# Kernel tuning notes

Measured on AMD Instinct MI355X. Metric: run time of the kernel, lower is better.

Reference implementation:

```python
import math
import jax, jax.numpy as jnp
import numpy as np


def setup_inputs() -> dict:
    key = jax.random.key(0)
    ks = jax.random.split(key, 6)
    B, L, d_model = 8, 4096, 512
    s = 1.0 / math.sqrt(d_model)
    inp = {
        "x": jax.random.normal(ks[0], (B, L, d_model), dtype=jnp.float32),
        "Wq": jax.random.normal(ks[1], (d_model, d_model), dtype=jnp.float32) * s,
        "bq": jnp.zeros((d_model,), jnp.float32),
        "Wk": jax.random.normal(ks[2], (d_model, d_model), dtype=jnp.float32) * s,
        "bk": jnp.zeros((d_model,), jnp.float32),
        "Wv": jax.random.normal(ks[3], (d_model, d_model), dtype=jnp.float32) * s,
        "bv": jnp.zeros((d_model,), jnp.float32),
        "Wo": jax.random.normal(ks[4], (d_model, d_model), dtype=jnp.float32) * s,
        "bo": jnp.zeros((d_model,), jnp.float32),
    }
    return inp


N_HEADS = 8
FACTOR = 1


def reference(x, Wq, bq, Wk, bk, Wv, bv, Wo, bo):
    B, L, d_model = x.shape
    H = N_HEADS
    D = d_model // H
    # projections (torch Linear: x @ W.T + b), reshape to (B,H,L,D)
    def proj(W, b):
        y = jnp.einsum("bld,ed->ble", x, W) + b
        return y.reshape(B, L, H, D).transpose(0, 2, 1, 3)
    q = proj(Wq, bq)
    k = proj(Wk, bk)
    v = proj(Wv, bv)
    # FFT autocorrelation along time axis (axis=2)
    q_f = jnp.fft.rfft(q, axis=2)
    k_f = jnp.fft.rfft(k, axis=2)
    corr = jnp.fft.irfft(q_f * jnp.conj(k_f), n=L, axis=2)  # (B,H,L,D)
    k_top = max(1, int(FACTOR * math.log(L + 1)))
    k_top = min(k_top, L)
    corr_mean = corr.mean(axis=-1)  # (B,H,L)
    top_vals, top_idx = jax.lax.top_k(corr_mean, k_top)  # (B,H,k)
    weights = jax.nn.softmax(top_vals, axis=-1)  # (B,H,k)
    t = jnp.arange(L).reshape(1, 1, 1, L)
    idx = (t + top_idx[..., None]) % L  # (B,H,k,L)
    # gather rolled V per selected lag: (B,H,k,L,D)
    v_exp = jnp.broadcast_to(v[:, :, None], (B, H, k_top, L, D))
    gathered = jnp.take_along_axis(v_exp, idx[..., None], axis=3)
    out = jnp.einsum("bhkld,bhk->bhld", gathered, weights)
    out = out.transpose(0, 2, 1, 3).reshape(B, L, d_model)
    # dropout=0.0 (eval): identity
    return jnp.einsum("bld,ed->ble", out, Wo) + bo
```

## Files before the change

kernel.cpp:

```cpp
#include <hip/hip_runtime.h>
#include <cstdint>
#include <cstddef>

#define AS1 __attribute__((address_space(1)))
#define AS3 __attribute__((address_space(3)))

using half8  = __attribute__((ext_vector_type(8))) _Float16;
using half4v = __attribute__((ext_vector_type(4))) _Float16;
using half2v = __attribute__((ext_vector_type(2))) _Float16;
using f32x4  = __attribute__((ext_vector_type(4))) float;

__global__ void prep_all_kernel(const float* __restrict__ x,
                                const float* __restrict__ Wq, const float* __restrict__ Wk,
                                const float* __restrict__ Wv, const float* __restrict__ Wo,
                                const float* __restrict__ bq, const float* __restrict__ bk,
                                const float* __restrict__ bv,
                                _Float16* __restrict__ xh, _Float16* __restrict__ Bt,
                                _Float16* __restrict__ WoH,
                                float2* __restrict__ tw, float* __restrict__ bias) {
    const int bid = blockIdx.x;
    const int tid = threadIdx.x;
    if (bid < 16384) {
        int i = (bid * 256 + tid) * 4;
        float4 v = *(const float4*)(x + i);
        half4v h;
        h[0] = (_Float16)v.x; h[1] = (_Float16)v.y;
        h[2] = (_Float16)v.z; h[3] = (_Float16)v.w;
        *(half4v*)(xh + i) = h;
    } else if (bid < 19456) {
        int i = (bid - 16384) * 256 + tid;
        int e = i >> 9, k = i & 511;
        int proj = e >> 9, er = e & 511;
        const float* W = (proj == 0) ? Wq : ((proj == 1) ? Wk : Wv);
        Bt[i] = (_Float16)W[er * 512 + k];
    } else if (bid < 20480) {
        int i = (bid - 19456) * 256 + tid;
        WoH[i] = (_Float16)Wo[i];
    } else if (bid < 20496) {
        int p = (bid - 20480) * 256 + tid;
        double th = -2.0 * 3.14159265358979323846 * (double)p / 4096.0;
        tw[p] = make_float2((float)cos(th), (float)sin(th));
    } else {
        int i = (bid - 20496) * 256 + tid;
        bias[i] = (i < 512) ? bq[i] : ((i < 1024) ? bk[i - 512] : bv[i - 1024]);
    }
}

template <int MODE>
__global__ __launch_bounds__(512, 2) void gemm_f16_kernel(
    const _Float16* __restrict__ A, const _Float16* __restrict__ Bt,
    const float* __restrict__ bias,
    _Float16* __restrict__ qT, _Float16* __restrict__ kT,
    _Float16* __restrict__ vout, float* __restrict__ Cout)
{
    constexpr int NBLK   = (MODE == 0) ? 6 : 2;
    constexpr int PERXCD = (MODE == 0) ? 96 : 32;
    __shared__ _Float16 smem[65536];

    const int gi = (blockIdx.x & 7) * PERXCD + (blockIdx.x >> 3);
    const int mb = gi / NBLK;
    const int nb = gi - mb * NBLK;
    const int m0 = mb * 256, n0 = nb * 256;
    const int tid = threadIdx.x;
    const int wave = tid >> 6, lane = tid & 63;
    const int lane15 = lane & 15, quad = lane >> 4;
    const int wmr = (wave >> 2) * 128;
    const int wnr = (wave & 3) * 64;

    const int r0 = tid >> 2;
    const int c0 = (tid & 3) ^ ((tid >> 3) & 3);
    const char* gA = (const char*)A  + ((size_t)(m0 + r0)) * 1024 + c0 * 16;
    const char* gB = (const char*)Bt + ((size_t)(n0 + r0)) * 1024 + c0 * 16;
    const int sbw = wave * 1024;
    const int coloff = (quad ^ ((lane15 >> 1) & 3)) << 4;

    f32x4 acc[8][4];
#pragma unroll
    for (int mi = 0; mi < 8; mi++)
#pragma unroll
        for (int ni = 0; ni < 4; ni++)
#pragma unroll
            for (int r = 0; r < 4; r++) acc[mi][ni][r] = 0.f;

    auto STAGE = [&](int slot, int tensor, int kk, int kt) {
        const char* g = (tensor == 0 ? gA : gB) + kt * 128 + kk * 64;
        char* base = (char*)smem + slot * 65536 + tensor * 32768 + kk * 16384 + sbw;
        __builtin_amdgcn_global_load_lds((const AS1 void*)g, (AS3 void*)base, 16, 0, 0);
        __builtin_amdgcn_global_load_lds((const AS1 void*)(g + 131072), (AS3 void*)(base + 8192), 16, 0, 0);
    };

    half8 af[4], bf[4];
    auto LOADA = [&](int slot, int kk, int mh) {
        const char* ba = (const char*)smem + slot * 65536 + kk * 16384;
#pragma unroll
        for (int j = 0; j < 4; j++)
            af[j] = *(const half8*)(ba + (wmr + (mh * 4 + j) * 16 + lane15) * 64 + coloff);
    };
    auto LOADB = [&](int slot, int kk) {
        const char* bb = (const char*)smem + slot * 65536 + 32768 + kk * 16384;
#pragma unroll
        for (int j = 0; j < 4; j++)
            bf[j] = *(const half8*)(bb + (wnr + j * 16 + lane15) * 64 + coloff);
    };
    auto MMA = [&](int mh) {
        __builtin_amdgcn_s_setprio(1);
#pragma unroll
        for (int j = 0; j < 4; j++)
#pragma unroll
            for (int ni = 0; ni < 4; ni++)
                acc[mh * 4 + j][ni] =
                    __builtin_amdgcn_mfma_f32_16x16x32_f16(af[j], bf[ni], acc[mh * 4 + j][ni], 0, 0, 0);
        __builtin_amdgcn_s_setprio(0);
    };
#define BAR() do { __builtin_amdgcn_s_barrier(); asm volatile("" ::: "memory"); } while (0)
#define VMW(n) asm volatile("s_waitcnt vmcnt(" #n ")" ::: "memory")

    STAGE(0, 0, 0, 0); STAGE(0, 1, 0, 0);
    STAGE(0, 0, 1, 0); STAGE(0, 1, 1, 0);
    STAGE(1, 0, 0, 1); STAGE(1, 1, 0, 1);
    VMW(8);
    BAR();

    for (int t = 0; t < 6; ++t) {
        const int slot = t & 1, nslot = slot ^ 1;
        LOADA(slot, 0, 0); LOADB(slot, 0);
        STAGE(nslot, 0, 1, t + 1);
        BAR(); MMA(0); BAR();
        LOADA(slot, 0, 1);
        STAGE(nslot, 1, 1, t + 1);
        BAR(); MMA(1);
        VMW(8);
        BAR();
        LOADA(slot, 1, 0); LOADB(slot, 1);
        STAGE(slot, 0, 0, t + 2);
        BAR(); MMA(0); BAR();
        LOADA(slot, 1, 1);
        STAGE(slot, 1, 0, t + 2);
        BAR(); MMA(1);
        VMW(8);
        BAR();
    }
    LOADA(0, 0, 0); LOADB(0, 0); STAGE(1, 0, 1, 7); BAR(); MMA(0); BAR();
    LOADA(0, 0, 1);              STAGE(1, 1, 1, 7); BAR(); MMA(1);
    VMW(8); BAR();
    LOADA(0, 1, 0); LOADB(0, 1); BAR(); MMA(0); BAR();
    LOADA(0, 1, 1);              BAR(); MMA(1);
    VMW(4);
    BAR();
    LOADA(1, 0, 0); LOADB(1, 0); BAR(); MMA(0); BAR();
    LOADA(1, 0, 1);              BAR(); MMA(1);
    VMW(0);
    BAR();
    LOADA(1, 1, 0); LOADB(1, 1); BAR(); MMA(0); BAR();
    LOADA(1, 1, 1);              BAR(); MMA(1);
#undef BAR
#undef VMW

    if (MODE == 1) {
#pragma unroll
        for (int mi = 0; mi < 8; mi++)
#pragma unroll
            for (int ni = 0; ni < 4; ni++) {
                const int n = n0 + wnr + ni * 16 + lane15;
                const float bb = bias[n];
#pragma unroll
                for (int r = 0; r < 4; r++) {
                    const int m = m0 + wmr + mi * 16 + quad * 4 + r;
                    Cout[(size_t)m * 512 + n] = acc[mi][ni][r] + bb;
                }
            }
        return;
    }
    const int proj = n0 >> 9;
    if (proj == 2) {
#pragma unroll
        for (int mi = 0; mi < 8; mi++)
#pragma unroll
            for (int ni = 0; ni < 4; ni++) {
                const int n = n0 + wnr + ni * 16 + lane15;
                const int er = n - 1024, h = er >> 6, d = er & 63;
                const float bb = bias[n];
#pragma unroll
                for (int r = 0; r < 4; r++) {
                    const int m = m0 + wmr + mi * 16 + quad * 4 + r;
                    const int b = m >> 12, l = m & 4095;
                    vout[((size_t)((b * 8 + h) * 4096 + l)) * 64 + d] = (_Float16)(acc[mi][ni][r] + bb);
                }
            }
        return;
    }
    _Float16* dst = (proj == 0) ? qT : kT;
    const int b = m0 >> 12;
    const int lbase = (m0 & 4095) + wmr + quad * 4;
#pragma unroll
    for (int mi = 0; mi < 8; mi++)
#pragma unroll
        for (int ni = 0; ni < 4; ni++) {
            const int e = n0 + wnr + ni * 16 + lane15;
            const int er = e & 511, h = er >> 6, d = er & 63;
            const float bb = bias[e];
            half4v o;
            o[0] = (_Float16)(acc[mi][ni][0] + bb);
            o[1] = (_Float16)(acc[mi][ni][1] + bb);
            o[2] = (_Float16)(acc[mi][ni][2] + bb);
            o[3] = (_Float16)(acc[mi][ni][3] + bb);
            *(half4v*)(dst + ((size_t)((b * 8 + h) * 64 + d)) * 4096 + lbase + mi * 16) = o;
        }
}

__device__ __forceinline__ float2 cmul(float2 a, float2 b) {
    return make_float2(a.x * b.x - a.y * b.y, a.x * b.y + a.y * b.x);
}
__device__ __forceinline__ float2 cmulc(float2 a, float cr, float ci) {
    return make_float2(a.x * cr - a.y * ci, a.x * ci + a.y * cr);
}
__device__ __forceinline__ int swz(int i) { return i ^ ((i >> 4) & 15); }

__device__ __forceinline__ void dft16(float2 x[16]) {
    constexpr float wc[10] = {1.f, 0.92387953f, 0.70710678f, 0.38268343f, 0.f,
                              0.f, -0.70710678f, 0.f, 0.f, -0.92387953f};
    constexpr float wsn[10] = {0.f, -0.38268343f, -0.70710678f, -0.92387953f, -1.f,
                               0.f, -0.70710678f, 0.f, 0.f, 0.38268343f};
    float2 t[16];
#pragma unroll
    for (int u = 0; u < 4; u++) {
        const float2 a = x[u], b = x[u + 4], c = x[u + 8], d = x[u + 12];
        const float2 Ea = make_float2(a.x + c.x, a.y + c.y);
        const float2 Oa = make_float2(a.x - c.x, a.y - c.y);
        const float2 Eb = make_float2(b.x + d.x, b.y + d.y);
        const float2 Ob = make_float2(b.x - d.x, b.y - d.y);
        const float2 y0 = make_float2(Ea.x + Eb.x, Ea.y + Eb.y);
        const float2 y1 = make_float2(Oa.x + Ob.y, Oa.y - Ob.x);
        const float2 y2 = make_float2(Ea.x - Eb.x, Ea.y - Eb.y);
        const float2 y3 = make_float2(Oa.x - Ob.y, Oa.y + Ob.x);
        t[4 * u + 0] = y0;
        t[4 * u + 1] = cmulc(y1, wc[u * 1], wsn[u * 1]);
        t[4 * u + 2] = cmulc(y2, wc[u * 2], wsn[u * 2]);
        t[4 * u + 3] = cmulc(y3, wc[u * 3], wsn[u * 3]);
    }
#pragma unroll
    for (int v = 0; v < 4; v++) {
        const float2 a = t[v], b = t[v + 4], c = t[v + 8], d = t[v + 12];
        const float2 Ea = make_float2(a.x + c.x, a.y + c.y);
        const float2 Oa = make_float2(a.x - c.x, a.y - c.y);
        const float2 Eb = make_float2(b.x + d.x, b.y + d.y);
        const float2 Ob = make_float2(b.x - d.x, b.y - d.y);
        x[v]      = make_float2(Ea.x + Eb.x, Ea.y + Eb.y);
        x[v + 4]  = make_float2(Oa.x + Ob.y, Oa.y - Ob.x);
        x[v + 8]  = make_float2(Ea.x - Eb.x, Ea.y - Eb.y);
        x[v + 12] = make_float2(Oa.x - Ob.y, Oa.y + Ob.x);
    }
}

__device__ __forceinline__ void fft4096_r16(float2* buf, const float2* __restrict__ tw,
                                            int tid, float2 (&x)[16]) {
    __syncthreads();
#pragma unroll
    for (int j = 0; j < 16; j++) x[j] = buf[swz(tid + 256 * j)];
    __syncthreads();
    dft16(x);
    buf[swz(16 * tid)] = x[0];
#pragma unroll
    for (int m = 1; m < 16; m++) buf[swz(16 * tid + m)] = cmul(x[m], tw[tid * m]);
    __syncthreads();
#pragma unroll
    for (int j = 0; j < 16; j++) x[j] = buf[swz(tid + 256 * j)];
    __syncthreads();
    dft16(x);
    {
        const int q = tid & 15, p = tid >> 4;
        const int base = q + 256 * p;
        buf[swz(base)] = x[0];
#pragma unroll
        for (int m = 1; m < 16; m++)
            buf[swz(base + 16 * m)] = cmul(x[m], tw[(p * m) << 4]);
    }
    __syncthreads();
#pragma unroll
    for (int j = 0; j < 16; j++) x[j] = buf[swz(tid + 256 * j)];
    __syncthreads();
    dft16(x);
#pragma unroll
    for (int m = 0; m < 16; m++) buf[swz(tid + 256 * m)] = x[m];
    __syncthreads();
}

__global__ __launch_bounds__(256) void fft_partial_kernel(
    const _Float16* __restrict__ qT, const _Float16* __restrict__ kT,
    const float2* __restrict__ tw, float2* __restrict__ spec)
{
    __shared__ float2 buf[4096];
    const int tid = threadIdx.x;
    const int bh = blockIdx.x >> 4, chunk = blockIdx.x & 15;
    float sx[16], sy[16];
#pragma unroll
    for (int i = 0; i < 16; i++) { sx[i] = 0.f; sy[i] = 0.f; }
    const _Float16* qb = qT + (size_t)bh * 64 * 4096;
    const _Float16* kb = kT + (size_t)bh * 64 * 4096;
    float2 x[16];
    for (int dd = 0; dd < 4; dd++) {
        const int d = chunk * 4 + dd;
#pragma unroll
        for (int i = 0; i < 2; i++) {
            const int t0 = 2048 * i + tid * 8;
            const half8 fq = *(const half8*)(qb + d * 4096 + t0);
            const half8 fk = *(const half8*)(kb + d * 4096 + t0);
#pragma unroll
            for (int j = 0; j < 8; j++)
                buf[swz(t0 + j)] = make_float2((float)fq[j], (float)fk[j]);
        }
        fft4096_r16(buf, tw, tid, x);
#pragma unroll
        for (int i = 0; i < 16; i++) {
            const int f = tid + 256 * i;
            const float2 Zf = x[i];
            const float2 Zm = buf[swz((4096 - f) & 4095)];
            const float Qr  = 0.5f * (Zf.x + Zm.x);
            const float Qi  = 0.5f * (Zf.y - Zm.y);
            const float cKr = 0.5f * (Zf.y + Zm.y);
            const float cKi = 0.5f * (Zf.x - Zm.x);
            sx[i] += Qr * cKr - Qi * cKi;
            sy[i] += Qr * cKi + Qi * cKr;
        }
        __syncthreads();
    }
    float2* out = spec + (size_t)blockIdx.x * 4096;
#pragma unroll
    for (int i = 0; i < 16; i++) out[tid + 256 * i] = make_float2(sx[i], sy[i]);
}

__global__ __launch_bounds__(256) void sum_spec_kernel(
    const float4* __restrict__ spec4, float4* __restrict__ ssum4)
{
    const int bh = blockIdx.x >> 3;
    const int i4 = (blockIdx.x & 7) * 256 + threadIdx.x;
    const float4* base = spec4 + (size_t)bh * 16 * 2048 + i4;
    float4 s = make_float4(0.f, 0.f, 0.f, 0.f);
#pragma unroll
    for (int c = 0; c < 16; c++) {
        const float4 v = base[(size_t)c * 2048];
        s.x += v.x; s.y += v.y; s.z += v.z; s.w += v.w;
    }
    s.y = -s.y; s.w = -s.w;
    ssum4[(size_t)bh * 2048 + i4] = s;
}

__global__ __launch_bounds__(256) void reduce_topk_kernel(
    const float2* __restrict__ ssum, const float2* __restrict__ tw,
    int* __restrict__ top_idx, float* __restrict__ top_w)
{
    __shared__ float2 buf[4096];
    __shared__ float wv[4];
    __shared__ int wi[4];
    const int tid = threadIdx.x;
    const int bh = blockIdx.x;
#pragma unroll
    for (int i = 0; i < 16; i++) {
        const int f = tid + 256 * i;
        buf[swz(f)] = ssum[(size_t)bh * 4096 + f];
    }
    float2 x[16];
    fft4096_r16(buf, tw, tid, x);
    float vals[8]; int idxs[8];
    for (int k = 0; k < 8; k++) {
        float best = -3.0e38f; int bi = 0;
#pragma unroll
        for (int i = 0; i < 16; i++) {
            const int f = tid + 256 * i;
            const float c = buf[swz(f)].x;
            if (c > best) { best = c; bi = f; }
        }
#pragma unroll
        for (int off = 32; off > 0; off >>= 1) {
            const float ov = __shfl_down(best, off);
            const int oi = __shfl_down(bi, off);
            if (ov > best || (ov == best && oi < bi)) { best = ov; bi = oi; }
        }
        if ((tid & 63) == 0) { wv[tid >> 6] = best; wi[tid >> 6] = bi; }
        __syncthreads();
        if (tid == 0) {
            best = wv[0]; bi = wi[0];
            for (int w = 1; w < 4; w++) {
                if (wv[w] > best || (wv[w] == best && wi[w] < bi)) { best = wv[w]; bi = wi[w]; }
            }
            vals[k] = best; idxs[k] = bi;
            buf[swz(bi)].x = -3.4e38f;
        }
        __syncthreads();
    }
    if (tid == 0) {
        const float scale = 1.f / (4096.f * 64.f);
        float e[8], s = 0.f;
        const float mx = vals[0] * scale;
        for (int k = 0; k < 8; k++) { e[k] = __expf(vals[k] * scale - mx); s += e[k]; }
        for (int k = 0; k < 8; k++) {
            top_w[bh * 8 + k] = e[k] / s;
            top_idx[bh * 8 + k] = idxs[k];
        }
    }
}

__global__ __launch_bounds__(256) void gather_kernel(
    const half8* __restrict__ v8, const int* __restrict__ top_idx,
    const float* __restrict__ top_w, half8* __restrict__ out8)
{
    const int gi = (blockIdx.x & 7) * 1024 + (blockIdx.x >> 3);
    const int bh = gi >> 7;
    const int lgrp = gi & 127;
    const int b = bh >> 3, h = bh & 7;
    const int tid = threadIdx.x;
    const int l = lgrp * 32 + (tid >> 3);
    const int d8 = tid & 7;
    int idx[8]; float w[8];
#pragma unroll
    for (int k = 0; k < 8; k++) { idx[k] = top_idx[bh * 8 + k]; w[k] = top_w[bh * 8 + k]; }
    const half8* vb = v8 + (size_t)bh * 4096 * 8;
    float a[8];
#pragma unroll
    for (int j = 0; j < 8; j++) a[j] = 0.f;
#pragma unroll
    for (int k = 0; k < 8; k++) {
        const int ls = (l + idx[k]) & 4095;
        const half8 pv = vb[(size_t)ls * 8 + d8];
#pragma unroll
        for (int j = 0; j < 8; j++) a[j] += w[k] * (float)pv[j];
    }
    half8 o;
#pragma unroll
    for (int j = 0; j < 8; j++) o[j] = (_Float16)a[j];
    out8[((size_t)(b * 4096 + l)) * 64 + h * 8 + d8] = o;
}

extern "C" void kernel_launch(void* const* d_in, const int* in_sizes, int n_in,
                              void* d_out, int out_size, void* d_ws, size_t ws_size,
                              hipStream_t stream) {
    (void)in_sizes; (void)n_in; (void)out_size; (void)ws_size;
    const float* x  = (const float*)d_in[0];
    const float* Wq = (const float*)d_in[1];
    const float* bq = (const float*)d_in[2];
    const float* Wk = (const float*)d_in[3];
    const float* bk = (const float*)d_in[4];
    const float* Wv = (const float*)d_in[5];
    const float* bv = (const float*)d_in[6];
    const float* Wo = (const float*)d_in[7];
    const float* bo = (const float*)d_in[8];
    float* out = (float*)d_out;

    char* ws = (char*)d_ws;
    size_t off = 0;
    auto alloc = [&](size_t bytes) -> void* {
        void* p = ws + off; off += (bytes + 255) & ~(size_t)255; return p;
    };
    _Float16* xh   = (_Float16*)alloc(33554432);
    _Float16* qT   = (_Float16*)alloc(33554432);
    _Float16* kT   = (_Float16*)alloc(33554432);
    _Float16* vbuf = (_Float16*)alloc(33554432);
    float2* spec   = (float2*)alloc(33554432);
    float2* ssum   = (float2*)alloc(2097152);
    _Float16* BtH  = (_Float16*)alloc(1572864);
    _Float16* WoH  = (_Float16*)alloc(524288);
    float* biasQKV = (float*)alloc(6144);
    float2* tw     = (float2*)alloc(32768);
    int*   top_idx = (int*)alloc(2048);
    float* top_w   = (float*)alloc(2048);
    _Float16* out_pre = xh;

    prep_all_kernel<<<20502, 256, 0, stream>>>(x, Wq, Wk, Wv, Wo, bq, bk, bv,
                                               xh, BtH, WoH, tw, biasQKV);
    gemm_f16_kernel<0><<<768, 512, 0, stream>>>(xh, BtH, biasQKV, qT, kT, vbuf, nullptr);
    fft_partial_kernel<<<1024, 256, 0, stream>>>(qT, kT, tw, spec);
    sum_spec_kernel<<<512, 256, 0, stream>>>((const float4*)spec, (float4*)ssum);
    reduce_topk_kernel<<<64, 256, 0, stream>>>(ssum, tw, top_idx, top_w);
    gather_kernel<<<8192, 256, 0, stream>>>((const half8*)vbuf, top_idx, top_w,
                                            (half8*)out_pre);
    gemm_f16_kernel<1><<<256, 512, 0, stream>>>(out_pre, WoH, bo, nullptr, nullptr, nullptr, out);
}
```

Baseline: 310.7 us.

## Make QKV GEMM persistent over three tiles, rework top-k, simplify gather mapping

The QKV projection GEMM now launches 256 blocks, and each block processes three output tiles in sequence. The next tile's first K-slices are prefetched into shared memory during the last iterations of the current tile, so the pipeline ramp-up between tiles is overlapped. Separately, the top-k selection keeps correlation values in registers, has each wave pick its own 8 candidates without block barriers, and merges the 32 candidates on one thread. The gather kernel also drops its XCD-interleaved block mapping. Running 256 persistent blocks may leave compute units idle compared with 768 blocks at two blocks per CU, and the epilogue stores are no longer overlapped with other blocks' compute.

New measurement: 327.0 us. 1.05x slower.

```diff
diff --git a/kernel.cpp b/kernel.cpp
--- a/kernel.cpp
+++ b/kernel.cpp
@@ -53,14 +53,10 @@
     _Float16* __restrict__ qT, _Float16* __restrict__ kT,
     _Float16* __restrict__ vout, float* __restrict__ Cout)
 {
-    constexpr int NBLK   = (MODE == 0) ? 6 : 2;
-    constexpr int PERXCD = (MODE == 0) ? 96 : 32;
+    constexpr int NBLKN = (MODE == 0) ? 6 : 2;
+    constexpr int NT    = (MODE == 0) ? 3 : 1;
     __shared__ _Float16 smem[65536];
 
-    const int gi = (blockIdx.x & 7) * PERXCD + (blockIdx.x >> 3);
-    const int mb = gi / NBLK;
-    const int nb = gi - mb * NBLK;
-    const int m0 = mb * 256, n0 = nb * 256;
     const int tid = threadIdx.x;
     const int wave = tid >> 6, lane = tid & 63;
     const int lane15 = lane & 15, quad = lane >> 4;
@@ -69,11 +65,25 @@
 
     const int r0 = tid >> 2;
     const int c0 = (tid & 3) ^ ((tid >> 3) & 3);
-    const char* gA = (const char*)A  + ((size_t)(m0 + r0)) * 1024 + c0 * 16;
-    const char* gB = (const char*)Bt + ((size_t)(n0 + r0)) * 1024 + c0 * 16;
     const int sbw = wave * 1024;
     const int coloff = (quad ^ ((lane15 >> 1) & 3)) << 4;
 
+    auto tileOf = [&](int j) -> int2 {
+        int gi;
+        if (MODE == 0) gi = (blockIdx.x & 7) * 96 + (blockIdx.x >> 3) * 3 + j;
+        else           gi = (blockIdx.x & 7) * 32 + (blockIdx.x >> 3);
+        const int mb = gi / NBLKN;
+        const int nb = gi - mb * NBLKN;
+        return make_int2(mb * 256, nb * 256);
+    };
+    auto mkA = [&](int m0) { return (const char*)A  + ((size_t)(m0 + r0)) * 1024 + c0 * 16; };
+    auto mkB = [&](int n0) { return (const char*)Bt + ((size_t)(n0 + r0)) * 1024 + c0 * 16; };
+
+    int2 cur = tileOf(0);
+    int2 nxt = tileOf(NT > 1 ? 1 : 0);
+    const char* gAc = mkA(cur.x); const char* gBc = mkB(cur.y);
+    const char* gAn = mkA(nxt.x); const char* gBn = mkB(nxt.y);
+
     f32x4 acc[8][4];
 #pragma unroll
     for (int mi = 0; mi < 8; mi++)
@@ -82,11 +92,11 @@
 #pragma unroll
             for (int r = 0; r < 4; r++) acc[mi][ni][r] = 0.f;
 
-    auto STAGE = [&](int slot, int tensor, int kk, int kt) {
-        const char* g = (tensor == 0 ? gA : gB) + kt * 128 + kk * 64;
+    auto STAGE = [&](int slot, const char* g, int tensor, int kk, int kt) {
+        const char* p = g + kt * 128 + kk * 64;
         char* base = (char*)smem + slot * 65536 + tensor * 32768 + kk * 16384 + sbw;
-        __builtin_amdgcn_global_load_lds((const AS1 void*)g, (AS3 void*)base, 16, 0, 0);
-        __builtin_amdgcn_global_load_lds((const AS1 void*)(g + 131072), (AS3 void*)(base + 8192), 16, 0, 0);
+        __builtin_amdgcn_global_load_lds((const AS1 void*)p, (AS3 void*)base, 16, 0, 0);
+        __builtin_amdgcn_global_load_lds((const AS1 void*)(p + 131072), (AS3 void*)(base + 8192), 16, 0, 0);
     };
 
     half8 af[4], bf[4];
@@ -115,97 +125,102 @@
 #define BAR() do { __builtin_amdgcn_s_barrier(); asm volatile("" ::: "memory"); } while (0)
 #define VMW(n) asm volatile("s_waitcnt vmcnt(" #n ")" ::: "memory")
 
-    STAGE(0, 0, 0, 0); STAGE(0, 1, 0, 0);
-    STAGE(0, 0, 1, 0); STAGE(0, 1, 1, 0);
-    STAGE(1, 0, 0, 1); STAGE(1, 1, 0, 1);
+    STAGE(0, gAc, 0, 0, 0); STAGE(0, gBc, 1, 0, 0);
+    STAGE(0, gAc, 0, 1, 0); STAGE(0, gBc, 1, 1, 0);
+    STAGE(1, gAc, 0, 0, 1); STAGE(1, gBc, 1, 0, 1);
     VMW(8);
     BAR();
 
-    for (int t = 0; t < 6; ++t) {
-        const int slot = t & 1, nslot = slot ^ 1;
-        LOADA(slot, 0, 0); LOADB(slot, 0);
-        STAGE(nslot, 0, 1, t + 1);
-        BAR(); MMA(0); BAR();
-        LOADA(slot, 0, 1);
-        STAGE(nslot, 1, 1, t + 1);
-        BAR(); MMA(1);
-        VMW(8);
-        BAR();
-        LOADA(slot, 1, 0); LOADB(slot, 1);
-        STAGE(slot, 0, 0, t + 2);
-        BAR(); MMA(0); BAR();
-        LOADA(slot, 1, 1);
-        STAGE(slot, 1, 0, t + 2);
-        BAR(); MMA(1);
-        VMW(8);
-        BAR();
-    }
-    LOADA(0, 0, 0); LOADB(0, 0); STAGE(1, 0, 1, 7); BAR(); MMA(0); BAR();
-    LOADA(0, 0, 1);              STAGE(1, 1, 1, 7); BAR(); MMA(1);
-    VMW(8); BAR();
-    LOADA(0, 1, 0); LOADB(0, 1); BAR(); MMA(0); BAR();
-    LOADA(0, 1, 1);              BAR(); MMA(1);
-    VMW(4);
-    BAR();
-    LOADA(1, 0, 0); LOADB(1, 0); BAR(); MMA(0); BAR();
-    LOADA(1, 0, 1);              BAR(); MMA(1);
-    VMW(0);
-    BAR();
-    LOADA(1, 1, 0); LOADB(1, 1); BAR(); MMA(0); BAR();
-    LOADA(1, 1, 1);              BAR(); MMA(1);
+    for (int j = 0; j < NT; ++j) {
+        for (int t = 0; t < 8; ++t) {
+            const int slot = t & 1, nslot = slot ^ 1;
+            const char* aF01 = (t < 7) ? gAc : gAn;
+            const char* bF01 = (t < 7) ? gBc : gBn;
+            const char* aF23 = (t < 6) ? gAc : gAn;
+            const char* bF23 = (t < 6) ? gBc : gBn;
+            const int k1 = (t + 1) & 7, k2 = (t + 2) & 7;
+            LOADA(slot, 0, 0); LOADB(slot, 0);
+            STAGE(nslot, aF01, 0, 1, k1);
+            BAR(); MMA(0); BAR();
+            LOADA(slot, 0, 1);
+            STAGE(nslot, bF01, 1, 1, k1);
+            BAR(); MMA(1);
+            VMW(8);
+            BAR();
+            LOADA(slot, 1, 0); LOADB(slot, 1);
+            STAGE(slot, aF23, 0, 0, k2);
+            BAR(); MMA(0); BAR();
+            LOADA(slot, 1, 1);
+            STAGE(slot, bF23, 1, 0, k2);
+            BAR(); MMA(1);
+            VMW(8);
+            BAR();
+        }
+        const int m0 = cur.x, n0 = cur.y;
+        if (MODE == 1) {
+#pragma unroll
+            for (int mi = 0; mi < 8; mi++)
+#pragma unroll
+                for (int ni = 0; ni < 4; ni++) {
+                    const int n = n0 + wnr + ni * 16 + lane15;
+                    const float bb = bias[n];
+#pragma unroll
+                    for (int r = 0; r < 4; r++) {
+                        const int m = m0 + wmr + mi * 16 + quad * 4 + r;
+                        Cout[(size_t)m * 512 + n] = acc[mi][ni][r] + bb;
+                    }
+                }
+        } else {
+            const int proj = n0 >> 9;
+            if (proj == 2) {
+#pragma unroll
+                for (int mi = 0; mi < 8; mi++)
+#pragma unroll
+                    for (int ni = 0; ni < 4; ni++) {
+                        const int n = n0 + wnr + ni * 16 + lane15;
+                        const int er = n - 1024, h = er >> 6, d = er & 63;
+                        const float bb = bias[n];
+#pragma unroll
+                        for (int r = 0; r < 4; r++) {
+                            const int m = m0 + wmr + mi * 16 + quad * 4 + r;
+                            const int b = m >> 12, l = m & 4095;
+                            vout[((size_t)((b * 8 + h) * 4096 + l)) * 64 + d] = (_Float16)(acc[mi][ni][r] + bb);
+                        }
+                    }
+            } else {
+                _Float16* dst = (proj == 0) ? qT : kT;
+                const int b = m0 >> 12;
+                const int lbase = (m0 & 4095) + wmr + quad * 4;
+#pragma unroll
+                for (int mi = 0; mi < 8; mi++)
+#pragma unroll
+                    for (int ni = 0; ni < 4; ni++) {
+                        const int e = n0 + wnr + ni * 16 + lane15;
+                        const int er = e & 511, h = er >> 6, d = er & 63;
+                        const float bb = bias[e];
+                        half4v o;
+                        o[0] = (_Float16)(acc[mi][ni][0] + bb);
+                        o[1] = (_Float16)(acc[mi][ni][1] + bb);
+                        o[2] = (_Float16)(acc[mi][ni][2] + bb);
+                        o[3] = (_Float16)(acc[mi][ni][3] + bb);
+                        *(half4v*)(dst + ((size_t)((b * 8 + h) * 64 + d)) * 4096 + lbase + mi * 16) = o;
+                    }
+            }
+        }
+        if (j + 1 < NT) {
+#pragma unroll
+            for (int mi = 0; mi < 8; mi++)
+#pragma unroll
+                for (int ni = 0; ni < 4; ni++)
+#pragma unroll
+                    for (int r = 0; r < 4; r++) acc[mi][ni][r] = 0.f;
+            cur = nxt; gAc = gAn; gBc = gBn;
+            const int2 nn = tileOf(j + 2 < NT ? j + 2 : 0);
+            nxt = nn; gAn = mkA(nn.x); gBn = mkB(nn.y);
+        }
+    }
 #undef BAR
 #undef VMW
-
-    if (MODE == 1) {
-#pragma unroll
-        for (int mi = 0; mi < 8; mi++)
-#pragma unroll
-            for (int ni = 0; ni < 4; ni++) {
-                const int n = n0 + wnr + ni * 16 + lane15;
-                const float bb = bias[n];
-#pragma unroll
-                for (int r = 0; r < 4; r++) {
-                    const int m = m0 + wmr + mi * 16 + quad * 4 + r;
-                    Cout[(size_t)m * 512 + n] = acc[mi][ni][r] + bb;
-                }
-            }
-        return;
-    }
-    const int proj = n0 >> 9;
-    if (proj == 2) {
-#pragma unroll
-        for (int mi = 0; mi < 8; mi++)
-#pragma unroll
-            for (int ni = 0; ni < 4; ni++) {
-                const int n = n0 + wnr + ni * 16 + lane15;
-                const int er = n - 1024, h = er >> 6, d = er & 63;
-                const float bb = bias[n];
-#pragma unroll
-                for (int r = 0; r < 4; r++) {
-                    const int m = m0 + wmr + mi * 16 + quad * 4 + r;
-                    const int b = m >> 12, l = m & 4095;
-                    vout[((size_t)((b * 8 + h) * 4096 + l)) * 64 + d] = (_Float16)(acc[mi][ni][r] + bb);
-                }
-            }
-        return;
-    }
-    _Float16* dst = (proj == 0) ? qT : kT;
-    const int b = m0 >> 12;
-    const int lbase = (m0 & 4095) + wmr + quad * 4;
-#pragma unroll
-    for (int mi = 0; mi < 8; mi++)
-#pragma unroll
-        for (int ni = 0; ni < 4; ni++) {
-            const int e = n0 + wnr + ni * 16 + lane15;
-            const int er = e & 511, h = er >> 6, d = er & 63;
-            const float bb = bias[e];
-            half4v o;
-            o[0] = (_Float16)(acc[mi][ni][0] + bb);
-            o[1] = (_Float16)(acc[mi][ni][1] + bb);
-            o[2] = (_Float16)(acc[mi][ni][2] + bb);
-            o[3] = (_Float16)(acc[mi][ni][3] + bb);
-            *(half4v*)(dst + ((size_t)((b * 8 + h) * 64 + d)) * 4096 + lbase + mi * 16) = o;
-        }
 }
 
 __device__ __forceinline__ float2 cmul(float2 a, float2 b) {
@@ -350,8 +365,8 @@
     int* __restrict__ top_idx, float* __restrict__ top_w)
 {
     __shared__ float2 buf[4096];
-    __shared__ float wv[4];
-    __shared__ int wi[4];
+    __shared__ float cval[32];
+    __shared__ int cidx[32];
     const int tid = threadIdx.x;
     const int bh = blockIdx.x;
 #pragma unroll
@@ -361,14 +376,16 @@
     }
     float2 x[16];
     fft4096_r16(buf, tw, tid, x);
-    float vals[8]; int idxs[8];
+    const int wid = tid >> 6;
+    float c[16];
+#pragma unroll
+    for (int i = 0; i < 16; i++) c[i] = buf[swz(tid + 256 * i)].x;
     for (int k = 0; k < 8; k++) {
         float best = -3.0e38f; int bi = 0;
 #pragma unroll
         for (int i = 0; i < 16; i++) {
             const int f = tid + 256 * i;
-            const float c = buf[swz(f)].x;
-            if (c > best) { best = c; bi = f; }
+            if (c[i] > best) { best = c[i]; bi = f; }
         }
 #pragma unroll
         for (int off = 32; off > 0; off >>= 1) {
@@ -376,19 +393,25 @@
             const int oi = __shfl_down(bi, off);
             if (ov > best || (ov == best && oi < bi)) { best = ov; bi = oi; }
         }
-        if ((tid & 63) == 0) { wv[tid >> 6] = best; wi[tid >> 6] = bi; }
-        __syncthreads();
-        if (tid == 0) {
-            best = wv[0]; bi = wi[0];
-            for (int w = 1; w < 4; w++) {
-                if (wv[w] > best || (wv[w] == best && wi[w] < bi)) { best = wv[w]; bi = wi[w]; }
+        best = __shfl(best, 0); bi = __shfl(bi, 0);
+        if ((tid & 63) == 0) { cval[wid * 8 + k] = best; cidx[wid * 8 + k] = bi; }
+        const int ii = bi >> 8;
+#pragma unroll
+        for (int i = 0; i < 16; i++)
+            if (i == ii && tid == (bi & 255)) c[i] = -3.4e38f;
+    }
+    __syncthreads();
+    if (tid == 0) {
+        float vals[8]; int idxs[8];
+        for (int k = 0; k < 8; k++) {
+            float best = -3.0e38f; int bi = 0; int bc = 0;
+            for (int cc = 0; cc < 32; cc++) {
+                const float v = cval[cc]; const int ix = cidx[cc];
+                if (v > best || (v == best && ix < bi)) { best = v; bi = ix; bc = cc; }
             }
+            cval[bc] = -3.4e38f;
             vals[k] = best; idxs[k] = bi;
-            buf[swz(bi)].x = -3.4e38f;
-        }
-        __syncthreads();
-    }
-    if (tid == 0) {
+        }
         const float scale = 1.f / (4096.f * 64.f);
         float e[8], s = 0.f;
         const float mx = vals[0] * scale;
@@ -404,9 +427,9 @@
     const half8* __restrict__ v8, const int* __restrict__ top_idx,
     const float* __restrict__ top_w, half8* __restrict__ out8)
 {
-    const int gi = (blockIdx.x & 7) * 1024 + (blockIdx.x >> 3);
-    const int bh = gi >> 7;
-    const int lgrp = gi & 127;
+    const int seq = blockIdx.x;
+    const int bh = seq >> 7;
+    const int lgrp = seq & 127;
     const int b = bh >> 3, h = bh & 7;
     const int tid = threadIdx.x;
     const int l = lgrp * 32 + (tid >> 3);
@@ -467,7 +490,7 @@
 
     prep_all_kernel<<<20502, 256, 0, stream>>>(x, Wq, Wk, Wv, Wo, bq, bk, bv,
                                                xh, BtH, WoH, tw, biasQKV);
-    gemm_f16_kernel<0><<<768, 512, 0, stream>>>(xh, BtH, biasQKV, qT, kT, vbuf, nullptr);
+    gemm_f16_kernel<0><<<256, 512, 0, stream>>>(xh, BtH, biasQKV, qT, kT, vbuf, nullptr);
     fft_partial_kernel<<<1024, 256, 0, stream>>>(qT, kT, tw, spec);
     sum_spec_kernel<<<512, 256, 0, stream>>>((const float4*)spec, (float4*)ssum);
     reduce_topk_kernel<<<64, 256, 0, stream>>>(ssum, tw, top_idx, top_w);
```

## Widen x conversion, register-resident top-k, and batch gather rows per block

Applied to the files above, without the earlier changes.

The x-to-half conversion now handles 8 elements per thread, halving the block count of the prep kernel. The top-k selection keeps each thread's 16 correlation values in registers and has each wave compute its own top-8 with no block barriers. Thread 0 then merges the 32 candidates. The gather kernel processes 4 row groups per block with 4x fewer blocks and drops the XCD-interleaved block mapping, which may change cache locality.

Result: slower. 351.1 us (+13.0%).

```diff
diff --git a/kernel.cpp b/kernel.cpp
--- a/kernel.cpp
+++ b/kernel.cpp
@@ -20,28 +20,31 @@
                                 float2* __restrict__ tw, float* __restrict__ bias) {
     const int bid = blockIdx.x;
     const int tid = threadIdx.x;
-    if (bid < 16384) {
-        int i = (bid * 256 + tid) * 4;
-        float4 v = *(const float4*)(x + i);
-        half4v h;
-        h[0] = (_Float16)v.x; h[1] = (_Float16)v.y;
-        h[2] = (_Float16)v.z; h[3] = (_Float16)v.w;
-        *(half4v*)(xh + i) = h;
-    } else if (bid < 19456) {
-        int i = (bid - 16384) * 256 + tid;
+    if (bid < 8192) {
+        int i = (bid * 256 + tid) * 8;
+        float4 v0 = *(const float4*)(x + i);
+        float4 v1 = *(const float4*)(x + i + 4);
+        half8 h;
+        h[0] = (_Float16)v0.x; h[1] = (_Float16)v0.y;
+        h[2] = (_Float16)v0.z; h[3] = (_Float16)v0.w;
+        h[4] = (_Float16)v1.x; h[5] = (_Float16)v1.y;
+        h[6] = (_Float16)v1.z; h[7] = (_Float16)v1.w;
+        *(half8*)(xh + i) = h;
+    } else if (bid < 11264) {
+        int i = (bid - 8192) * 256 + tid;
         int e = i >> 9, k = i & 511;
         int proj = e >> 9, er = e & 511;
         const float* W = (proj == 0) ? Wq : ((proj == 1) ? Wk : Wv);
         Bt[i] = (_Float16)W[er * 512 + k];
-    } else if (bid < 20480) {
-        int i = (bid - 19456) * 256 + tid;
+    } else if (bid < 12288) {
+        int i = (bid - 11264) * 256 + tid;
         WoH[i] = (_Float16)Wo[i];
-    } else if (bid < 20496) {
-        int p = (bid - 20480) * 256 + tid;
+    } else if (bid < 12304) {
+        int p = (bid - 12288) * 256 + tid;
         double th = -2.0 * 3.14159265358979323846 * (double)p / 4096.0;
         tw[p] = make_float2((float)cos(th), (float)sin(th));
     } else {
-        int i = (bid - 20496) * 256 + tid;
+        int i = (bid - 12304) * 256 + tid;
         bias[i] = (i < 512) ? bq[i] : ((i < 1024) ? bk[i - 512] : bv[i - 1024]);
     }
 }
@@ -350,8 +353,8 @@
     int* __restrict__ top_idx, float* __restrict__ top_w)
 {
     __shared__ float2 buf[4096];
-    __shared__ float wv[4];
-    __shared__ int wi[4];
+    __shared__ float cval[32];
+    __shared__ int cidx[32];
     const int tid = threadIdx.x;
     const int bh = blockIdx.x;
 #pragma unroll
@@ -361,14 +364,16 @@
     }
     float2 x[16];
     fft4096_r16(buf, tw, tid, x);
-    float vals[8]; int idxs[8];
+    const int wid = tid >> 6;
+    float c[16];
+#pragma unroll
+    for (int i = 0; i < 16; i++) c[i] = buf[swz(tid + 256 * i)].x;
     for (int k = 0; k < 8; k++) {
         float best = -3.0e38f; int bi = 0;
 #pragma unroll
         for (int i = 0; i < 16; i++) {
             const int f = tid + 256 * i;
-            const float c = buf[swz(f)].x;
-            if (c > best) { best = c; bi = f; }
+            if (c[i] > best) { best = c[i]; bi = f; }
         }
 #pragma unroll
         for (int off = 32; off > 0; off >>= 1) {
@@ -376,19 +381,25 @@
             const int oi = __shfl_down(bi, off);
             if (ov > best || (ov == best && oi < bi)) { best = ov; bi = oi; }
         }
-        if ((tid & 63) == 0) { wv[tid >> 6] = best; wi[tid >> 6] = bi; }
-        __syncthreads();
-        if (tid == 0) {
-            best = wv[0]; bi = wi[0];
-            for (int w = 1; w < 4; w++) {
-                if (wv[w] > best || (wv[w] == best && wi[w] < bi)) { best = wv[w]; bi = wi[w]; }
+        best = __shfl(best, 0); bi = __shfl(bi, 0);
+        if ((tid & 63) == 0) { cval[wid * 8 + k] = best; cidx[wid * 8 + k] = bi; }
+        const int ii = bi >> 8;
+#pragma unroll
+        for (int i = 0; i < 16; i++)
+            if (i == ii && tid == (bi & 255)) c[i] = -3.4e38f;
+    }
+    __syncthreads();
+    if (tid == 0) {
+        float vals[8]; int idxs[8];
+        for (int k = 0; k < 8; k++) {
+            float best = -3.0e38f; int bi = 0; int bc = 0;
+            for (int cc = 0; cc < 32; cc++) {
+                const float v = cval[cc]; const int ix = cidx[cc];
+                if (v > best || (v == best && ix < bi)) { best = v; bi = ix; bc = cc; }
             }
+            cval[bc] = -3.4e38f;
             vals[k] = best; idxs[k] = bi;
-            buf[swz(bi)].x = -3.4e38f;
-        }
-        __syncthreads();
-    }
-    if (tid == 0) {
+        }
         const float scale = 1.f / (4096.f * 64.f);
         float e[8], s = 0.f;
         const float mx = vals[0] * scale;
@@ -404,31 +415,34 @@
     const half8* __restrict__ v8, const int* __restrict__ top_idx,
     const float* __restrict__ top_w, half8* __restrict__ out8)
 {
-    const int gi = (blockIdx.x & 7) * 1024 + (blockIdx.x >> 3);
-    const int bh = gi >> 7;
-    const int lgrp = gi & 127;
+    const int bh = blockIdx.x >> 5;
     const int b = bh >> 3, h = bh & 7;
     const int tid = threadIdx.x;
-    const int l = lgrp * 32 + (tid >> 3);
     const int d8 = tid & 7;
     int idx[8]; float w[8];
 #pragma unroll
     for (int k = 0; k < 8; k++) { idx[k] = top_idx[bh * 8 + k]; w[k] = top_w[bh * 8 + k]; }
     const half8* vb = v8 + (size_t)bh * 4096 * 8;
-    float a[8];
-#pragma unroll
-    for (int j = 0; j < 8; j++) a[j] = 0.f;
-#pragma unroll
-    for (int k = 0; k < 8; k++) {
-        const int ls = (l + idx[k]) & 4095;
-        const half8 pv = vb[(size_t)ls * 8 + d8];
-#pragma unroll
-        for (int j = 0; j < 8; j++) a[j] += w[k] * (float)pv[j];
-    }
-    half8 o;
-#pragma unroll
-    for (int j = 0; j < 8; j++) o[j] = (_Float16)a[j];
-    out8[((size_t)(b * 4096 + l)) * 64 + h * 8 + d8] = o;
+#pragma unroll
+    for (int it = 0; it < 4; ++it) {
+        const int seq = blockIdx.x * 4 + it;
+        const int lgrp = seq & 127;
+        const int l = lgrp * 32 + (tid >> 3);
+        float a[8];
+#pragma unroll
+        for (int j = 0; j < 8; j++) a[j] = 0.f;
+#pragma unroll
+        for (int k = 0; k < 8; k++) {
+            const int ls = (l + idx[k]) & 4095;
+            const half8 pv = vb[(size_t)ls * 8 + d8];
+#pragma unroll
+            for (int j = 0; j < 8; j++) a[j] += w[k] * (float)pv[j];
+        }
+        half8 o;
+#pragma unroll
+        for (int j = 0; j < 8; j++) o[j] = (_Float16)a[j];
+        out8[((size_t)(b * 4096 + l)) * 64 + h * 8 + d8] = o;
+    }
 }
 
 extern "C" void kernel_launch(void* const* d_in, const int* in_sizes, int n_in,
@@ -465,13 +479,13 @@
     float* top_w   = (float*)alloc(2048);
     _Float16* out_pre = xh;
 
-    prep_all_kernel<<<20502, 256, 0, stream>>>(x, Wq, Wk, Wv, Wo, bq, bk, bv,
+    prep_all_kernel<<<12310, 256, 0, stream>>>(x, Wq, Wk, Wv, Wo, bq, bk, bv,
                                                xh, BtH, WoH, tw, biasQKV);
     gemm_f16_kernel<0><<<768, 512, 0, stream>>>(xh, BtH, biasQKV, qT, kT, vbuf, nullptr);
     fft_partial_kernel<<<1024, 256, 0, stream>>>(qT, kT, tw, spec);
     sum_spec_kernel<<<512, 256, 0, stream>>>((const float4*)spec, (float4*)ssum);
     reduce_topk_kernel<<<64, 256, 0, stream>>>(ssum, tw, top_idx, top_w);
-    gather_kernel<<<8192, 256, 0, stream>>>((const half8*)vbuf, top_idx, top_w,
+    gather_kernel<<<2048, 256, 0, stream>>>((const half8*)vbuf, top_idx, top_w,
                                             (half8*)out_pre);
     gemm_f16_kernel<1><<<256, 512, 0, stream>>>(out_pre, WoH, bo, nullptr, nullptr, nullptr, out);
 }
```
